# Optimization experiments

Hardware: AMD Instinct MI355X
Metric: run time of the kernel (lower is better)

## Reference

```python
import jax, jax.numpy as jnp
import numpy as np

NUM_HEADS = 16
EPS = 1e-6
CHUNK = 128  # chunk length for exact chunked-recurrent causal linear attention


def setup_inputs() -> dict:
    key = jax.random.key(0)
    ks = jax.random.split(key, 6)
    B, T, E = 4, 2048, 1024
    s = 0.02
    x = jax.random.normal(ks[0], (B, T, E), jnp.float32)
    Wq = jax.random.normal(ks[1], (E, E), jnp.float32) * s
    Wk = jax.random.normal(ks[2], (E, E), jnp.float32) * s
    Wv = jax.random.normal(ks[3], (E, E), jnp.float32) * s
    Wp = jax.random.normal(ks[4], (E, E), jnp.float32) * s
    bp = jnp.zeros((E,), jnp.float32)
    return {"x": x, "Wq": Wq, "Wk": Wk, "Wv": Wv, "Wp": Wp, "bp": bp}


def reference(x, Wq, Wk, Wv, Wp, bp):
    B, T, E = x.shape
    H = NUM_HEADS
    D = E // H
    N = T // CHUNK

    q = x @ Wq.T
    k = x @ Wk.T
    v = x @ Wv.T

    def split_heads(t):  # [B,T,E] -> [B,H,N,C,D]
        return t.reshape(B, T, H, D).transpose(0, 2, 1, 3).reshape(B, H, N, CHUNK, D)

    phi_q = jax.nn.elu(split_heads(q)) + 1.0
    phi_k = jax.nn.elu(split_heads(k)) + 1.0
    vh = split_heads(v)

    # per-chunk KV state and key-sum, then exclusive prefix over chunks
    kv = jnp.einsum('bhncd,bhnce->bhnde', phi_k, vh)        # [B,H,N,D,D]
    zk = phi_k.sum(axis=3)                                   # [B,H,N,D]
    S_prev = jnp.concatenate(
        [jnp.zeros_like(kv[:, :, :1]), jnp.cumsum(kv, axis=2)[:, :, :-1]], axis=2)
    Z_prev = jnp.concatenate(
        [jnp.zeros_like(zk[:, :, :1]), jnp.cumsum(zk, axis=2)[:, :, :-1]], axis=2)

    # intra-chunk causal part
    A = jnp.einsum('bhncd,bhnsd->bhncs', phi_q, phi_k)       # [B,H,N,C,C]
    mask = jnp.tril(jnp.ones((CHUNK, CHUNK), bool))
    A = jnp.where(mask, A, 0.0)

    num = (jnp.einsum('bhncs,bhnse->bhnce', A, vh)
           + jnp.einsum('bhncd,bhnde->bhnce', phi_q, S_prev))
    den = A.sum(-1) + jnp.einsum('bhncd,bhnd->bhnc', phi_q, Z_prev) + EPS
    y = num / den[..., None]                                  # [B,H,N,C,D]

    y = y.reshape(B, H, T, D).transpose(0, 2, 1, 3).reshape(B, T, E)
    return y @ Wp.T + bp
```

## Files before the change

kernel.cpp:

```cpp
#include <hip/hip_runtime.h>
#include <hip/hip_bf16.h>
#include <stdint.h>

#define T_LEN  2048
#define E_DIM  1024
#define BATCH  4
#define HEADS  16
#define HDIM   64
#define CHUNK_ 128
#define NCHUNK 16
#define EPS_   1e-6f

typedef __attribute__((ext_vector_type(8))) short bf16x8;
typedef __attribute__((ext_vector_type(4))) float f32x4;

__device__ __forceinline__ float b2f(__hip_bfloat16 h) { return __bfloat162float(h); }
__device__ __forceinline__ unsigned short f2bu(float f) {
  __hip_bfloat16 h = __float2bfloat16(f);
  return *(unsigned short*)&h;
}
__device__ __forceinline__ void gld_lds16(const void* g, void* l) {
  __builtin_amdgcn_global_load_lds((const __attribute__((address_space(1))) void*)g,
                                   (__attribute__((address_space(3))) void*)l,
                                   16, 0, 0);
}

__global__ __launch_bounds__(256)
void cast5(const float* __restrict__ x,  const float* __restrict__ w0,
           const float* __restrict__ w1, const float* __restrict__ w2,
           const float* __restrict__ w3,
           __hip_bfloat16* __restrict__ xb,  __hip_bfloat16* __restrict__ w0b,
           __hip_bfloat16* __restrict__ w1b, __hip_bfloat16* __restrict__ w2b,
           __hip_bfloat16* __restrict__ w3b)
{
  const int b = blockIdx.x;
  const float* s;
  __hip_bfloat16* d;
  size_t off;
  if (b < 8192) { s = x; d = xb; off = (size_t)b * 1024; }
  else {
    const int i = (b - 8192) >> 10;
    const int r = (b - 8192) & 1023;
    s = (i == 0) ? w0 : (i == 1) ? w1 : (i == 2) ? w2 : w3;
    d = (i == 0) ? w0b : (i == 1) ? w1b : (i == 2) ? w2b : w3b;
    off = (size_t)r * 1024;
  }
  const int t = threadIdx.x;
  float4 v = *(const float4*)(s + off + (size_t)t * 4);
  ushort4 o;
  o.x = f2bu(v.x); o.y = f2bu(v.y); o.z = f2bu(v.z); o.w = f2bu(v.w);
  *(ushort4*)((unsigned short*)d + off + (size_t)t * 4) = o;
}

__device__ __forceinline__ void gemm128_core(
    const __hip_bfloat16* __restrict__ X,
    const __hip_bfloat16* __restrict__ W,
    int bm, int bn, f32x4 acc[4][4],
    __hip_bfloat16* Xs, __hip_bfloat16* Ws)
{
  const int t = threadIdx.x, lane = t & 63, wave = t >> 6;
  const int wm = (wave >> 1) * 64, wn = (wave & 1) * 64;
  for (int k0 = 0; k0 < 1024; k0 += 32) {
    if (k0) __syncthreads();
#pragma unroll
    for (int i = 0; i < 2; ++i) {
      const int j = wave * 2 + i;
      const int m = j * 16 + (lane >> 2);
      const int kg = lane & 3;
      gld_lds16(X + (size_t)(bm * 128 + m) * 1024 + k0 + kg * 8, (char*)Xs + j * 1024);
      gld_lds16(W + (size_t)(bn * 128 + m) * 1024 + k0 + kg * 8, (char*)Ws + j * 1024);
    }
    __syncthreads();
    bf16x8 a[4], b[4];
#pragma unroll
    for (int i = 0; i < 4; ++i) {
      a[i] = *(const bf16x8*)&Xs[((wm + i * 16 + (lane & 15)) * 4 + (lane >> 4)) * 8];
      b[i] = *(const bf16x8*)&Ws[((wn + i * 16 + (lane & 15)) * 4 + (lane >> 4)) * 8];
    }
#pragma unroll
    for (int i = 0; i < 4; ++i)
#pragma unroll
      for (int jn = 0; jn < 4; ++jn)
        acc[i][jn] = __builtin_amdgcn_mfma_f32_16x16x32_bf16(a[i], b[jn], acc[i][jn], 0, 0, 0);
  }
}

__global__ __launch_bounds__(256, 2)
void gemm_qkv(const __hip_bfloat16* __restrict__ X,
              const __hip_bfloat16* __restrict__ Wq,
              const __hip_bfloat16* __restrict__ Wk,
              const __hip_bfloat16* __restrict__ Wv,
              __hip_bfloat16* __restrict__ qo,
              __hip_bfloat16* __restrict__ ko,
              __hip_bfloat16* __restrict__ vo)
{
  __shared__ __align__(16) __hip_bfloat16 Xs[128 * 32];
  __shared__ __align__(16) __hip_bfloat16 Ws[128 * 32];
  const int bm = blockIdx.x, bnx = blockIdx.y;
  const int which = bnx >> 3, bn = bnx & 7;
  const __hip_bfloat16* W = (which == 0) ? Wq : (which == 1) ? Wk : Wv;
  __hip_bfloat16* C = (which == 0) ? qo : (which == 1) ? ko : vo;
  const bool elu = (which < 2);
  f32x4 acc[4][4];
#pragma unroll
  for (int i = 0; i < 4; ++i)
#pragma unroll
    for (int j = 0; j < 4; ++j) acc[i][j] = (f32x4){0.f, 0.f, 0.f, 0.f};
  gemm128_core(X, W, bm, bn, acc, Xs, Ws);
  const int lane = threadIdx.x & 63, wave = threadIdx.x >> 6;
  const int wm = (wave >> 1) * 64, wn = (wave & 1) * 64;
  const int r0 = (lane >> 4) * 4;
#pragma unroll
  for (int mi = 0; mi < 4; ++mi)
#pragma unroll
    for (int ni = 0; ni < 4; ++ni) {
      const int row = bm * 128 + wm + mi * 16 + r0;
      const int col = bn * 128 + wn + ni * 16 + (lane & 15);
#pragma unroll
      for (int r = 0; r < 4; ++r) {
        float v = acc[mi][ni][r];
        if (elu) v = (v > 0.f) ? (v + 1.f) : __expf(v);
        C[(size_t)(row + r) * 1024 + col] = __float2bfloat16(v);
      }
    }
}

__global__ __launch_bounds__(256, 2)
void gemm_out(const __hip_bfloat16* __restrict__ X,
              const __hip_bfloat16* __restrict__ W,
              const float* __restrict__ bias,
              float* __restrict__ C)
{
  __shared__ __align__(16) __hip_bfloat16 Xs[128 * 32];
  __shared__ __align__(16) __hip_bfloat16 Ws[128 * 32];
  const int bm = blockIdx.x, bn = blockIdx.y;
  f32x4 acc[4][4];
#pragma unroll
  for (int i = 0; i < 4; ++i)
#pragma unroll
    for (int j = 0; j < 4; ++j) acc[i][j] = (f32x4){0.f, 0.f, 0.f, 0.f};
  gemm128_core(X, W, bm, bn, acc, Xs, Ws);
  const int lane = threadIdx.x & 63, wave = threadIdx.x >> 6;
  const int wm = (wave >> 1) * 64, wn = (wave & 1) * 64;
  const int r0 = (lane >> 4) * 4;
#pragma unroll
  for (int mi = 0; mi < 4; ++mi)
#pragma unroll
    for (int ni = 0; ni < 4; ++ni) {
      const int row = bm * 128 + wm + mi * 16 + r0;
      const int col = bn * 128 + wn + ni * 16 + (lane & 15);
      const float bv = bias[col];
#pragma unroll
      for (int r = 0; r < 4; ++r)
        C[(size_t)(row + r) * 1024 + col] = acc[mi][ni][r] + bv;
    }
}

__global__ __launch_bounds__(256)
void chunk_kv(const __hip_bfloat16* __restrict__ Kp,
              const __hip_bfloat16* __restrict__ Vp,
              float* __restrict__ kvout, float* __restrict__ zkout,
              unsigned short* __restrict__ vimg)
{
  const int bid = blockIdx.x;
  const int n = bid & 15, h = (bid >> 4) & 15, b = bid >> 8;
  __shared__ __align__(16) __hip_bfloat16 ks[CHUNK_ * HDIM];
  __shared__ __align__(16) __hip_bfloat16 vs[CHUNK_ * HDIM];
  const size_t base = ((size_t)(b * T_LEN + n * CHUNK_)) * E_DIM + h * HDIM;
  const int t = threadIdx.x;
  for (int i = t; i < CHUNK_ * 8; i += 256) {
    int r = i >> 3, c = (i & 7) << 3;
    *(uint4*)&ks[r * HDIM + c] = *(const uint4*)(Kp + base + (size_t)r * E_DIM + c);
    *(uint4*)&vs[r * HDIM + c] = *(const uint4*)(Vp + base + (size_t)r * E_DIM + c);
  }
  __syncthreads();
  const int d0 = (t >> 4) << 2, e0 = (t & 15) << 2;
  float acc[4][4] = {{0.f}};
  float z[4] = {0.f, 0.f, 0.f, 0.f};
  for (int c = 0; c < CHUNK_; ++c) {
    float kv4[4], vv4[4];
#pragma unroll
    for (int i = 0; i < 4; ++i) kv4[i] = b2f(ks[c * HDIM + d0 + i]);
#pragma unroll
    for (int j = 0; j < 4; ++j) vv4[j] = b2f(vs[c * HDIM + e0 + j]);
#pragma unroll
    for (int i = 0; i < 4; ++i) {
      z[i] += kv4[i];
#pragma unroll
      for (int j = 0; j < 4; ++j) acc[i][j] += kv4[i] * vv4[j];
    }
  }
  float* o = kvout + (size_t)bid * (HDIM * HDIM);
  const int dg = d0 >> 3, doff = d0 & 7;
#pragma unroll
  for (int i = 0; i < 4; ++i)
#pragma unroll
    for (int j = 0; j < 4; ++j)
      o[dg * 512 + (e0 + j) * 8 + doff + i] = acc[i][j];
  if (e0 == 0) {
#pragma unroll
    for (int i = 0; i < 4; ++i) zkout[(size_t)bid * HDIM + d0 + i] = z[i];
  }
  const unsigned short* vsu = (const unsigned short*)vs;
  unsigned short* vo = vimg + (size_t)bid * 8192;
  for (int slot = t; slot < 1024; slot += 256) {
    const int sg = slot >> 6, e = slot & 63;
    ushort4 lo, hi;
    lo.x = vsu[(sg * 8 + 0) * 64 + e]; lo.y = vsu[(sg * 8 + 1) * 64 + e];
    lo.z = vsu[(sg * 8 + 2) * 64 + e]; lo.w = vsu[(sg * 8 + 3) * 64 + e];
    hi.x = vsu[(sg * 8 + 4) * 64 + e]; hi.y = vsu[(sg * 8 + 5) * 64 + e];
    hi.z = vsu[(sg * 8 + 6) * 64 + e]; hi.w = vsu[(sg * 8 + 7) * 64 + e];
    *(ushort4*)&vo[slot * 8] = lo;
    *(ushort4*)&vo[slot * 8 + 4] = hi;
  }
}

__global__ __launch_bounds__(256)
void prefix_chunks(float* __restrict__ S, float* __restrict__ Z)
{
  const int bh = blockIdx.x;
  const int t = threadIdx.x;
  float run[16];
#pragma unroll
  for (int j = 0; j < 16; ++j) run[j] = 0.f;
  for (int n = 0; n < NCHUNK; ++n) {
    float* p = S + ((size_t)bh * NCHUNK + n) * (HDIM * HDIM);
#pragma unroll
    for (int j = 0; j < 16; ++j) {
      int idx = t + j * 256;
      float cur = p[idx];
      p[idx] = run[j];
      run[j] += cur;
    }
  }
  if (t < HDIM) {
    float rz = 0.f;
    for (int n = 0; n < NCHUNK; ++n) {
      float* p = Z + ((size_t)bh * NCHUNK + n) * HDIM + t;
      float cur = *p;
      *p = rz;
      rz += cur;
    }
  }
}

#define PW_STRIDE 136

__global__ __launch_bounds__(256, 3)
void chunk_attn(const __hip_bfloat16* __restrict__ Qp,
                const __hip_bfloat16* __restrict__ Kp,
                const unsigned short* __restrict__ vimg,
                const float* __restrict__ Simg,
                const float* __restrict__ Zp,
                __hip_bfloat16* __restrict__ Yp)
{
  __shared__ __align__(16) unsigned short VL[8192];
  __shared__ __align__(16) unsigned short SL[4096];
  __shared__ __align__(16) unsigned short PL[4 * 16 * PW_STRIDE];

  const int bid = blockIdx.x;
  const int n = bid & 15, h = (bid >> 4) & 15, b = bid >> 8;
  const int tokbase = b * T_LEN + n * CHUNK_;
  const size_t gbase = (size_t)tokbase * E_DIM + h * HDIM;
  const int t = threadIdx.x, lane = t & 63, wv = t >> 6;
  const int lm = lane & 15, kg = lane >> 4;

#pragma unroll
  for (int i = 0; i < 4; ++i) {
    const int j = wv * 4 + i;
    gld_lds16(vimg + (size_t)bid * 8192 + (size_t)(j * 64 + lane) * 8,
              (char*)VL + j * 1024);
  }
#pragma unroll
  for (int i = 0; i < 4; ++i) {
    const int idx = i * 1024 + t * 4;
    float4 s4 = *(const float4*)(Simg + (size_t)bid * 4096 + idx);
    ushort4 o;
    o.x = f2bu(s4.x); o.y = f2bu(s4.y); o.z = f2bu(s4.z); o.w = f2bu(s4.w);
    *(ushort4*)&SL[idx] = o;
  }

  const int mts[2] = { wv, 7 - wv };
  bf16x8 aq[2][2];
#pragma unroll
  for (int mi = 0; mi < 2; ++mi)
#pragma unroll
    for (int kh = 0; kh < 2; ++kh)
      aq[mi][kh] = *(const bf16x8*)(Qp + gbase +
                    (size_t)(mts[mi] * 16 + lm) * E_DIM + kh * 32 + kg * 8);
  bf16x8 zb[2];
#pragma unroll
  for (int kh = 0; kh < 2; ++kh) {
    float4 z0 = *(const float4*)(Zp + (size_t)bid * 64 + kh * 32 + kg * 8);
    float4 z1 = *(const float4*)(Zp + (size_t)bid * 64 + kh * 32 + kg * 8 + 4);
    zb[kh][0] = (short)f2bu(z0.x); zb[kh][1] = (short)f2bu(z0.y);
    zb[kh][2] = (short)f2bu(z0.z); zb[kh][3] = (short)f2bu(z0.w);
    zb[kh][4] = (short)f2bu(z1.x); zb[kh][5] = (short)f2bu(z1.y);
    zb[kh][6] = (short)f2bu(z1.z); zb[kh][7] = (short)f2bu(z1.w);
  }

  __syncthreads();

  f32x4 accn[2][4];
  f32x4 accden[2];
#pragma unroll
  for (int mi = 0; mi < 2; ++mi) {
    accden[mi] = (f32x4){EPS_, EPS_, EPS_, EPS_};
#pragma unroll
    for (int ne = 0; ne < 4; ++ne) accn[mi][ne] = (f32x4){0.f, 0.f, 0.f, 0.f};
  }

#pragma unroll
  for (int mi = 0; mi < 2; ++mi)
#pragma unroll
    for (int kh = 0; kh < 2; ++kh) {
      const bf16x8 a = aq[mi][kh];
      accden[mi] = __builtin_amdgcn_mfma_f32_16x16x32_bf16(a, zb[kh], accden[mi], 0, 0, 0);
#pragma unroll
      for (int ne = 0; ne < 4; ++ne) {
        bf16x8 bs = *(const bf16x8*)&SL[((kh * 4 + kg) * 64 + ne * 16 + lm) * 8];
        accn[mi][ne] = __builtin_amdgcn_mfma_f32_16x16x32_bf16(a, bs, accn[mi][ne], 0, 0, 0);
      }
    }

  unsigned short* Pw = PL + wv * 16 * PW_STRIDE;
  bf16x8 ones;
#pragma unroll
  for (int j = 0; j < 8; ++j) ones[j] = (short)0x3F80;

#pragma unroll
  for (int mi = 0; mi < 2; ++mi) {
    const int mt = mts[mi], m0 = mt * 16;
    for (int nt = 0; nt <= mt; ++nt) {
      f32x4 pt = (f32x4){0.f, 0.f, 0.f, 0.f};
#pragma unroll
      for (int kh = 0; kh < 2; ++kh) {
        bf16x8 ak = *(const bf16x8*)(Kp + gbase +
                     (size_t)(nt * 16 + lm) * E_DIM + kh * 32 + kg * 8);
        pt = __builtin_amdgcn_mfma_f32_16x16x32_bf16(ak, aq[mi][kh], pt, 0, 0, 0);
      }
      unsigned short u[4];
#pragma unroll
      for (int r = 0; r < 4; ++r) {
        float v = pt[r];
        if (nt == mt) {
          v = ((kg * 4 + r) <= lm) ? v : 0.f;
        }
        u[r] = f2bu(v);
      }
      const int sidx = lm * PW_STRIDE + nt * 16 + kg * 4;
      *(unsigned*)&Pw[sidx]     = (unsigned)u[0] | ((unsigned)u[1] << 16);
      *(unsigned*)&Pw[sidx + 2] = (unsigned)u[2] | ((unsigned)u[3] << 16);
    }
    if ((mt & 1) == 0 && lane < 32) {
      const int m = lane >> 1, half = lane & 1;
      *(uint4*)&Pw[m * PW_STRIDE + (mt + 1) * 16 + half * 8] = (uint4){0u, 0u, 0u, 0u};
    }
    const int ktc = (mt + 2) >> 1;
    for (int kt = 0; kt < ktc; ++kt) {
      bf16x8 ap = *(const bf16x8*)&Pw[lm * PW_STRIDE + kt * 32 + kg * 8];
      accden[mi] = __builtin_amdgcn_mfma_f32_16x16x32_bf16(ap, ones, accden[mi], 0, 0, 0);
#pragma unroll
      for (int ne = 0; ne < 4; ++ne) {
        bf16x8 bv = *(const bf16x8*)&VL[((kt * 4 + kg) * 64 + ne * 16 + lm) * 8];
        accn[mi][ne] = __builtin_amdgcn_mfma_f32_16x16x32_bf16(ap, bv, accn[mi][ne], 0, 0, 0);
      }
    }
  }

#pragma unroll
  for (int mi = 0; mi < 2; ++mi) {
    const int m0 = mts[mi] * 16;
    float inv[4];
#pragma unroll
    for (int r = 0; r < 4; ++r) inv[r] = 1.f / accden[mi][r];
#pragma unroll
    for (int ne = 0; ne < 4; ++ne) {
      const int col = h * HDIM + ne * 16 + lm;
#pragma unroll
      for (int r = 0; r < 4; ++r) {
        const int row = tokbase + m0 + kg * 4 + r;
        Yp[(size_t)row * E_DIM + col] = __float2bfloat16(accn[mi][ne][r] * inv[r]);
      }
    }
  }
}

extern "C" void kernel_launch(void* const* d_in, const int* in_sizes, int n_in,
                              void* d_out, int out_size, void* d_ws, size_t ws_size,
                              hipStream_t stream)
{
  const float* x  = (const float*)d_in[0];
  const float* Wq = (const float*)d_in[1];
  const float* Wk = (const float*)d_in[2];
  const float* Wv = (const float*)d_in[3];
  const float* Wp = (const float*)d_in[4];
  const float* bp = (const float*)d_in[5];
  float* out = (float*)d_out;

  const size_t MT = (size_t)BATCH * T_LEN;
  char* w = (char*)d_ws;
  __hip_bfloat16* xb  = (__hip_bfloat16*)w; w += MT * E_DIM * sizeof(__hip_bfloat16);
  __hip_bfloat16* Wqb = (__hip_bfloat16*)w; w += (size_t)E_DIM * E_DIM * sizeof(__hip_bfloat16);
  __hip_bfloat16* Wkb = (__hip_bfloat16*)w; w += (size_t)E_DIM * E_DIM * sizeof(__hip_bfloat16);
  __hip_bfloat16* Wvb = (__hip_bfloat16*)w; w += (size_t)E_DIM * E_DIM * sizeof(__hip_bfloat16);
  __hip_bfloat16* Wpb = (__hip_bfloat16*)w; w += (size_t)E_DIM * E_DIM * sizeof(__hip_bfloat16);
  __hip_bfloat16* q = (__hip_bfloat16*)w; w += MT * E_DIM * sizeof(__hip_bfloat16);
  __hip_bfloat16* k = (__hip_bfloat16*)w; w += MT * E_DIM * sizeof(__hip_bfloat16);
  __hip_bfloat16* v = (__hip_bfloat16*)w; w += MT * E_DIM * sizeof(__hip_bfloat16);
  __hip_bfloat16* y = (__hip_bfloat16*)w; w += MT * E_DIM * sizeof(__hip_bfloat16);
  float* S = (float*)w; w += (size_t)BATCH * HEADS * NCHUNK * HDIM * HDIM * sizeof(float);
  float* Z = (float*)w; w += (size_t)BATCH * HEADS * NCHUNK * HDIM * sizeof(float);
  unsigned short* vimg = (unsigned short*)xb;

  cast5<<<8192 + 4096, 256, 0, stream>>>(x, Wq, Wk, Wv, Wp, xb, Wqb, Wkb, Wvb, Wpb);
  gemm_qkv<<<dim3(MT / 128, 24), 256, 0, stream>>>(xb, Wqb, Wkb, Wvb, q, k, v);
  chunk_kv<<<BATCH * HEADS * NCHUNK, 256, 0, stream>>>(k, v, S, Z, vimg);
  prefix_chunks<<<BATCH * HEADS, 256, 0, stream>>>(S, Z);
  chunk_attn<<<BATCH * HEADS * NCHUNK, 256, 0, stream>>>(q, k, vimg, S, Z, y);
  gemm_out<<<dim3(MT / 128, 8), 256, 0, stream>>>(y, Wpb, bp, out);
}
```

Before: 246.7 us.

## Replace QKV GEMM with 256x256-tile double-buffered pipelined MFMA kernel

Replaces the 128x128-tile QKV projection GEMM with a 512-thread kernel using 256x256 output tiles and BK=64. It double-buffers LDS with swizzled layouts, interleaves quarter-tile global-to-LDS loads with MFMA phases using explicit vmcnt waits and barriers, and raises wave priority during MFMA blocks. The aim is more data reuse per tile and hiding global load latency behind compute. The cost is 128KB of LDS per block and fewer blocks (384) to spread across the CUs.

New measurement: 260.0 us. 5.4% more time.

```diff
diff --git a/kernel.cpp b/kernel.cpp
--- a/kernel.cpp
+++ b/kernel.cpp
@@ -85,44 +85,207 @@
   }
 }
 
-__global__ __launch_bounds__(256, 2)
-void gemm_qkv(const __hip_bfloat16* __restrict__ X,
-              const __hip_bfloat16* __restrict__ Wq,
-              const __hip_bfloat16* __restrict__ Wk,
-              const __hip_bfloat16* __restrict__ Wv,
-              __hip_bfloat16* __restrict__ qo,
-              __hip_bfloat16* __restrict__ ko,
-              __hip_bfloat16* __restrict__ vo)
-{
-  __shared__ __align__(16) __hip_bfloat16 Xs[128 * 32];
-  __shared__ __align__(16) __hip_bfloat16 Ws[128 * 32];
-  const int bm = blockIdx.x, bnx = blockIdx.y;
-  const int which = bnx >> 3, bn = bnx & 7;
-  const __hip_bfloat16* W = (which == 0) ? Wq : (which == 1) ? Wk : Wv;
+__global__ __launch_bounds__(512, 2)
+void gemm_qkv_256(const __hip_bfloat16* __restrict__ X,
+                  const __hip_bfloat16* __restrict__ Wq,
+                  const __hip_bfloat16* __restrict__ Wk,
+                  const __hip_bfloat16* __restrict__ Wv,
+                  __hip_bfloat16* __restrict__ qo,
+                  __hip_bfloat16* __restrict__ ko,
+                  __hip_bfloat16* __restrict__ vo)
+{
+  __shared__ __align__(16) unsigned short As[2][16384];
+  __shared__ __align__(16) unsigned short Bs[2][16384];
+
+  const int bm = blockIdx.x;
+  const int byy = blockIdx.y;
+  const int which = byy >> 2, bn = byy & 3;
+  const __hip_bfloat16* Wsel = (which == 0) ? Wq : (which == 1) ? Wk : Wv;
   __hip_bfloat16* C = (which == 0) ? qo : (which == 1) ? ko : vo;
   const bool elu = (which < 2);
-  f32x4 acc[4][4];
-#pragma unroll
-  for (int i = 0; i < 4; ++i)
-#pragma unroll
-    for (int j = 0; j < 4; ++j) acc[i][j] = (f32x4){0.f, 0.f, 0.f, 0.f};
-  gemm128_core(X, W, bm, bn, acc, Xs, Ws);
-  const int lane = threadIdx.x & 63, wave = threadIdx.x >> 6;
-  const int wm = (wave >> 1) * 64, wn = (wave & 1) * 64;
+
+  const int t = threadIdx.x, lane = t & 63, wv = t >> 6;
+  const int wm = (wv >> 2) * 128;
+  const int wn = (wv & 3) * 64;
+
+  const __hip_bfloat16* Xp = X + (size_t)(bm * 256) * 1024;
+  const __hip_bfloat16* Wp = Wsel + (size_t)(bn * 256) * 1024;
+
+  const int lo    = (lane & 15) * 128;
+  const int lohi0 = lo + (((lane >> 4)    ) ^ (lane & 7)) * 16;
+  const int lohi1 = lo + (((lane >> 4) | 4) ^ (lane & 7)) * 16;
+
+  auto stage_half = [&](int jn, int c) {
+    if (jn >= 16) return;
+    const int buf = jn & 1;
+    const int k0 = jn * 64;
+#pragma unroll
+    for (int ci = 0; ci < 2; ++ci) {
+      const int i = wv * 2 + ci;
+      int row0;
+      const __hip_bfloat16* G;
+      char* L;
+      if (c == 0)      { row0 = (i & 7) * 8 + (i >> 3) * 128;      G = Xp; L = (char*)&As[buf][0]; }
+      else if (c == 2) { row0 = 64 + (i & 7) * 8 + (i >> 3) * 128; G = Xp; L = (char*)&As[buf][0]; }
+      else if (c == 1) { row0 = (i & 3) * 8 + (i >> 2) * 64;       G = Wp; L = (char*)&Bs[buf][0]; }
+      else             { row0 = 32 + (i & 3) * 8 + (i >> 2) * 64;  G = Wp; L = (char*)&Bs[buf][0]; }
+      const int row = row0 + (lane >> 3);
+      const int cg  = (lane & 7) ^ (lane >> 3);
+      gld_lds16(G + (size_t)row * 1024 + k0 + cg * 8, L + row0 * 128);
+    }
+  };
+
+  auto vmw = [&](int n) {
+    if (n == 6)      asm volatile("s_waitcnt vmcnt(6)" ::: "memory");
+    else if (n == 4) asm volatile("s_waitcnt vmcnt(4)" ::: "memory");
+    else if (n == 2) asm volatile("s_waitcnt vmcnt(2)" ::: "memory");
+    else             asm volatile("s_waitcnt vmcnt(0)" ::: "memory");
+  };
+
+  f32x4 acc[8][4];
+#pragma unroll
+  for (int m = 0; m < 8; ++m)
+#pragma unroll
+    for (int n = 0; n < 4; ++n) acc[m][n] = (f32x4){0.f, 0.f, 0.f, 0.f};
+
+  bf16x8 a0[4][2], a1[4][2], b0[2][2], b1[2][2];
+  {
+    bf16x8 zz;
+#pragma unroll
+    for (int i = 0; i < 8; ++i) zz[i] = (short)0;
+#pragma unroll
+    for (int m = 0; m < 4; ++m) { a1[m][0] = zz; a1[m][1] = zz; }
+#pragma unroll
+    for (int n = 0; n < 2; ++n) { b1[n][0] = zz; b1[n][1] = zz; }
+  }
+
+  stage_half(0, 0); stage_half(0, 1); stage_half(0, 2); stage_half(0, 3);
+  vmw(6);
+  __builtin_amdgcn_s_barrier();
+
+  auto kstep = [&](int j, int buf, bool last) {
+    const char* Ab = (const char*)&As[buf][0];
+    const char* Bb = (const char*)&Bs[buf][0];
+    const int jn = j + 1;
+
+#pragma unroll
+    for (int m = 0; m < 4; ++m) {
+      a0[m][0] = *(const bf16x8*)(Ab + (wm + m * 16) * 128 + lohi0);
+      a0[m][1] = *(const bf16x8*)(Ab + (wm + m * 16) * 128 + lohi1);
+    }
+    stage_half(jn, 0);
+    __builtin_amdgcn_s_barrier();
+    asm volatile("s_waitcnt lgkmcnt(0)" ::: "memory");
+    __builtin_amdgcn_sched_barrier(0);
+    __builtin_amdgcn_s_setprio(1);
+#pragma unroll
+    for (int m = 0; m < 4; ++m)
+#pragma unroll
+      for (int n = 0; n < 2; ++n) {
+        acc[4 + m][2 + n] = __builtin_amdgcn_mfma_f32_16x16x32_bf16(a1[m][0], b1[n][0], acc[4 + m][2 + n], 0, 0, 0);
+        acc[4 + m][2 + n] = __builtin_amdgcn_mfma_f32_16x16x32_bf16(a1[m][1], b1[n][1], acc[4 + m][2 + n], 0, 0, 0);
+      }
+    __builtin_amdgcn_s_setprio(0);
+    vmw(last ? 4 : 6);
+    __builtin_amdgcn_s_barrier();
+
+#pragma unroll
+    for (int n = 0; n < 2; ++n) {
+      b0[n][0] = *(const bf16x8*)(Bb + (wn + n * 16) * 128 + lohi0);
+      b0[n][1] = *(const bf16x8*)(Bb + (wn + n * 16) * 128 + lohi1);
+    }
+    stage_half(jn, 1);
+    __builtin_amdgcn_s_barrier();
+    asm volatile("s_waitcnt lgkmcnt(0)" ::: "memory");
+    __builtin_amdgcn_sched_barrier(0);
+    __builtin_amdgcn_s_setprio(1);
+#pragma unroll
+    for (int m = 0; m < 4; ++m)
+#pragma unroll
+      for (int n = 0; n < 2; ++n) {
+        acc[m][n] = __builtin_amdgcn_mfma_f32_16x16x32_bf16(a0[m][0], b0[n][0], acc[m][n], 0, 0, 0);
+        acc[m][n] = __builtin_amdgcn_mfma_f32_16x16x32_bf16(a0[m][1], b0[n][1], acc[m][n], 0, 0, 0);
+      }
+    __builtin_amdgcn_s_setprio(0);
+    vmw(last ? 2 : 6);
+    __builtin_amdgcn_s_barrier();
+
+#pragma unroll
+    for (int m = 0; m < 4; ++m) {
+      a1[m][0] = *(const bf16x8*)(Ab + (wm + 64 + m * 16) * 128 + lohi0);
+      a1[m][1] = *(const bf16x8*)(Ab + (wm + 64 + m * 16) * 128 + lohi1);
+    }
+    stage_half(jn, 2);
+    __builtin_amdgcn_s_barrier();
+    asm volatile("s_waitcnt lgkmcnt(0)" ::: "memory");
+    __builtin_amdgcn_sched_barrier(0);
+    __builtin_amdgcn_s_setprio(1);
+#pragma unroll
+    for (int m = 0; m < 4; ++m)
+#pragma unroll
+      for (int n = 0; n < 2; ++n) {
+        acc[4 + m][n] = __builtin_amdgcn_mfma_f32_16x16x32_bf16(a1[m][0], b0[n][0], acc[4 + m][n], 0, 0, 0);
+        acc[4 + m][n] = __builtin_amdgcn_mfma_f32_16x16x32_bf16(a1[m][1], b0[n][1], acc[4 + m][n], 0, 0, 0);
+      }
+    __builtin_amdgcn_s_setprio(0);
+    vmw(last ? 0 : 6);
+    __builtin_amdgcn_s_barrier();
+
+#pragma unroll
+    for (int n = 0; n < 2; ++n) {
+      b1[n][0] = *(const bf16x8*)(Bb + (wn + 32 + n * 16) * 128 + lohi0);
+      b1[n][1] = *(const bf16x8*)(Bb + (wn + 32 + n * 16) * 128 + lohi1);
+    }
+    stage_half(jn, 3);
+    __builtin_amdgcn_s_barrier();
+    asm volatile("s_waitcnt lgkmcnt(0)" ::: "memory");
+    __builtin_amdgcn_sched_barrier(0);
+    __builtin_amdgcn_s_setprio(1);
+#pragma unroll
+    for (int m = 0; m < 4; ++m)
+#pragma unroll
+      for (int n = 0; n < 2; ++n) {
+        acc[m][2 + n] = __builtin_amdgcn_mfma_f32_16x16x32_bf16(a0[m][0], b1[n][0], acc[m][2 + n], 0, 0, 0);
+        acc[m][2 + n] = __builtin_amdgcn_mfma_f32_16x16x32_bf16(a0[m][1], b1[n][1], acc[m][2 + n], 0, 0, 0);
+      }
+    __builtin_amdgcn_s_setprio(0);
+    if (!last) {
+      vmw(6);
+      __builtin_amdgcn_s_barrier();
+    }
+  };
+
+#pragma unroll 1
+  for (int jj = 0; jj < 7; ++jj) {
+    kstep(2 * jj,     0, false);
+    kstep(2 * jj + 1, 1, false);
+  }
+  kstep(14, 0, false);
+  kstep(15, 1, true);
+
+#pragma unroll
+  for (int m = 0; m < 4; ++m)
+#pragma unroll
+    for (int n = 0; n < 2; ++n) {
+      acc[4 + m][2 + n] = __builtin_amdgcn_mfma_f32_16x16x32_bf16(a1[m][0], b1[n][0], acc[4 + m][2 + n], 0, 0, 0);
+      acc[4 + m][2 + n] = __builtin_amdgcn_mfma_f32_16x16x32_bf16(a1[m][1], b1[n][1], acc[4 + m][2 + n], 0, 0, 0);
+    }
+
   const int r0 = (lane >> 4) * 4;
 #pragma unroll
-  for (int mi = 0; mi < 4; ++mi)
-#pragma unroll
-    for (int ni = 0; ni < 4; ++ni) {
-      const int row = bm * 128 + wm + mi * 16 + r0;
-      const int col = bn * 128 + wn + ni * 16 + (lane & 15);
+  for (int m = 0; m < 8; ++m) {
+    const int row = bm * 256 + wm + m * 16 + r0;
+#pragma unroll
+    for (int n = 0; n < 4; ++n) {
+      const int col = bn * 256 + wn + n * 16 + (lane & 15);
 #pragma unroll
       for (int r = 0; r < 4; ++r) {
-        float v = acc[mi][ni][r];
-        if (elu) v = (v > 0.f) ? (v + 1.f) : __expf(v);
-        C[(size_t)(row + r) * 1024 + col] = __float2bfloat16(v);
-      }
-    }
+        float vv = acc[m][n][r];
+        if (elu) vv = (vv > 0.f) ? (vv + 1.f) : __expf(vv);
+        C[(size_t)(row + r) * 1024 + col] = __float2bfloat16(vv);
+      }
+    }
+  }
 }
 
 __global__ __launch_bounds__(256, 2)
@@ -414,7 +577,7 @@
   unsigned short* vimg = (unsigned short*)xb;
 
   cast5<<<8192 + 4096, 256, 0, stream>>>(x, Wq, Wk, Wv, Wp, xb, Wqb, Wkb, Wvb, Wpb);
-  gemm_qkv<<<dim3(MT / 128, 24), 256, 0, stream>>>(xb, Wqb, Wkb, Wvb, q, k, v);
+  gemm_qkv_256<<<dim3(32, 12), 512, 0, stream>>>(xb, Wqb, Wkb, Wvb, q, k, v);
   chunk_kv<<<BATCH * HEADS * NCHUNK, 256, 0, stream>>>(k, v, S, Z, vimg);
   prefix_chunks<<<BATCH * HEADS, 256, 0, stream>>>(S, Z);
   chunk_attn<<<BATCH * HEADS * NCHUNK, 256, 0, stream>>>(q, k, vimg, S, Z, y);
```

## Rewrite QKV GEMM with 128x256 tiles, triple-buffered LDS pipeline and swizzle

Applied to the files above, without the earlier changes.

Replaces the QKV projection GEMM with a 512-thread kernel that computes 128x256 output tiles with a K-step of 64. Global-to-LDS loads go into three LDS buffers and are interleaved between MFMA groups, with explicit vmcnt waits, s_setprio and register double-buffering of fragments. An XOR swizzle on the LDS layout is meant to avoid bank conflicts. The goal is to hide memory latency and raise MFMA utilisation, at the cost of heavy LDS use (about 144KB) and a single block per CU.

After: 245.6 us. Within noise of the previous version (-0.4%).

```diff
diff --git a/kernel.cpp b/kernel.cpp
--- a/kernel.cpp
+++ b/kernel.cpp
@@ -24,6 +24,8 @@
                                    (__attribute__((address_space(3))) void*)l,
                                    16, 0, 0);
 }
+
+#define MFMA16(a, b, c) __builtin_amdgcn_mfma_f32_16x16x32_bf16((a), (b), (c), 0, 0, 0)
 
 __global__ __launch_bounds__(256)
 void cast5(const float* __restrict__ x,  const float* __restrict__ w0,
@@ -81,48 +83,187 @@
     for (int i = 0; i < 4; ++i)
 #pragma unroll
       for (int jn = 0; jn < 4; ++jn)
-        acc[i][jn] = __builtin_amdgcn_mfma_f32_16x16x32_bf16(a[i], b[jn], acc[i][jn], 0, 0, 0);
-  }
-}
-
-__global__ __launch_bounds__(256, 2)
-void gemm_qkv(const __hip_bfloat16* __restrict__ X,
-              const __hip_bfloat16* __restrict__ Wq,
-              const __hip_bfloat16* __restrict__ Wk,
-              const __hip_bfloat16* __restrict__ Wv,
-              __hip_bfloat16* __restrict__ qo,
-              __hip_bfloat16* __restrict__ ko,
-              __hip_bfloat16* __restrict__ vo)
-{
-  __shared__ __align__(16) __hip_bfloat16 Xs[128 * 32];
-  __shared__ __align__(16) __hip_bfloat16 Ws[128 * 32];
-  const int bm = blockIdx.x, bnx = blockIdx.y;
-  const int which = bnx >> 3, bn = bnx & 7;
-  const __hip_bfloat16* W = (which == 0) ? Wq : (which == 1) ? Wk : Wv;
-  __hip_bfloat16* C = (which == 0) ? qo : (which == 1) ? ko : vo;
+        acc[i][jn] = MFMA16(a[i], b[jn], acc[i][jn]);
+  }
+}
+
+__global__ __launch_bounds__(512, 1)
+void gemm_qkv_v2(const __hip_bfloat16* __restrict__ X,
+                 const __hip_bfloat16* __restrict__ Wq,
+                 const __hip_bfloat16* __restrict__ Wk,
+                 const __hip_bfloat16* __restrict__ Wv,
+                 __hip_bfloat16* __restrict__ qo,
+                 __hip_bfloat16* __restrict__ ko,
+                 __hip_bfloat16* __restrict__ vo)
+{
+  __shared__ __align__(16) unsigned short As[3][8192];
+  __shared__ __align__(16) unsigned short Bs[3][16384];
+
+  const int bm = blockIdx.x;
+  const int byy = blockIdx.y;
+  const int which = byy >> 2, bn = byy & 3;
+  const __hip_bfloat16* Wsel = (which == 0) ? Wq : (which == 1) ? Wk : Wv;
+  __hip_bfloat16* Cc = (which == 0) ? qo : (which == 1) ? ko : vo;
   const bool elu = (which < 2);
+
+  const int t = threadIdx.x, lane = t & 63, wv = t >> 6;
+  const int wm = (wv >> 2) * 64;
+  const int wn = (wv & 3) * 64;
+
+  const __hip_bfloat16* Xp = X + (size_t)(bm * 128) * 1024;
+  const __hip_bfloat16* Wp = Wsel + (size_t)(bn * 256) * 1024;
+
+  const int lo    = (lane & 15) * 128;
+  const int lohi0 = lo + (((lane >> 4)    ) ^ (lane & 7)) * 16;
+  const int lohi1 = lo + (((lane >> 4) | 4) ^ (lane & 7)) * 16;
+  const int srow = lane >> 3;
+  const int scg  = (lane & 7) ^ (lane >> 3);
+
+  auto stA = [&](int buf, int k0) {
+#pragma unroll
+    for (int ci = 0; ci < 2; ++ci) {
+      const int row0 = (wv * 2 + ci) * 8;
+      gld_lds16(Xp + (size_t)(row0 + srow) * 1024 + k0 + scg * 8,
+                (char*)&As[buf][0] + row0 * 128);
+    }
+  };
+  auto stB0 = [&](int buf, int k0) {
+#pragma unroll
+    for (int ci = 0; ci < 2; ++ci) {
+      const int row0 = (wv * 2 + ci) * 8;
+      gld_lds16(Wp + (size_t)(row0 + srow) * 1024 + k0 + scg * 8,
+                (char*)&Bs[buf][0] + row0 * 128);
+    }
+  };
+  auto stB1 = [&](int buf, int k0) {
+#pragma unroll
+    for (int ci = 0; ci < 2; ++ci) {
+      const int row0 = 128 + (wv * 2 + ci) * 8;
+      gld_lds16(Wp + (size_t)(row0 + srow) * 1024 + k0 + scg * 8,
+                (char*)&Bs[buf][0] + row0 * 128);
+    }
+  };
+  auto rdA = [&](int buf, int half, bf16x8 (&d)[2][2]) {
+#pragma unroll
+    for (int m = 0; m < 2; ++m) {
+      const int rb = wm + half * 32 + m * 16;
+      d[m][0] = *(const bf16x8*)((const char*)&As[buf][0] + rb * 128 + lohi0);
+      d[m][1] = *(const bf16x8*)((const char*)&As[buf][0] + rb * 128 + lohi1);
+    }
+  };
+  auto rdB = [&](int buf, int half, bf16x8 (&d)[2][2]) {
+#pragma unroll
+    for (int n = 0; n < 2; ++n) {
+      const int rb = wn + half * 32 + n * 16;
+      d[n][0] = *(const bf16x8*)((const char*)&Bs[buf][0] + rb * 128 + lohi0);
+      d[n][1] = *(const bf16x8*)((const char*)&Bs[buf][0] + rb * 128 + lohi1);
+    }
+  };
+
   f32x4 acc[4][4];
 #pragma unroll
-  for (int i = 0; i < 4; ++i)
-#pragma unroll
-    for (int j = 0; j < 4; ++j) acc[i][j] = (f32x4){0.f, 0.f, 0.f, 0.f};
-  gemm128_core(X, W, bm, bn, acc, Xs, Ws);
-  const int lane = threadIdx.x & 63, wave = threadIdx.x >> 6;
-  const int wm = (wave >> 1) * 64, wn = (wave & 1) * 64;
+  for (int m = 0; m < 4; ++m)
+#pragma unroll
+    for (int n = 0; n < 4; ++n) acc[m][n] = (f32x4){0.f, 0.f, 0.f, 0.f};
+
+  bf16x8 Aa01[2][2], Ab01[2][2], Aa23[2][2], Ab23[2][2];
+  bf16x8 Ba01[2][2], Bb01[2][2], Ba23[2][2], Bb23[2][2];
+
+  stA(0, 0);  stB0(0, 0);  stB1(0, 0);
+  stA(1, 64); stB0(1, 64); stB1(1, 64);
+  asm volatile("s_waitcnt vmcnt(6)" ::: "memory");
+  __builtin_amdgcn_s_barrier();
+  __builtin_amdgcn_sched_barrier(0);
+  rdA(0, 0, Aa01); rdB(0, 0, Ab01); rdA(0, 1, Aa23); rdB(0, 1, Ab23);
+
+  auto qstep = [&](int j, int c,
+                   bf16x8 (&ca01)[2][2], bf16x8 (&cb01)[2][2],
+                   bf16x8 (&ca23)[2][2], bf16x8 (&cb23)[2][2],
+                   bf16x8 (&na01)[2][2], bf16x8 (&nb01)[2][2],
+                   bf16x8 (&na23)[2][2], bf16x8 (&nb23)[2][2]) {
+    const int stg  = (c + 2 >= 3) ? c - 1 : c + 2;
+    const int nbuf = (c + 1 >= 3) ? 0 : c + 1;
+    const int k0n  = (j + 2) * 64;
+    const bool dost = (j < 14);
+
+    __builtin_amdgcn_s_setprio(1);
+#pragma unroll
+    for (int m = 0; m < 2; ++m)
+#pragma unroll
+      for (int n = 0; n < 2; ++n) {
+        acc[m][n] = MFMA16(ca01[m][0], cb01[n][0], acc[m][n]);
+        acc[m][n] = MFMA16(ca01[m][1], cb01[n][1], acc[m][n]);
+      }
+    __builtin_amdgcn_s_setprio(0);
+    if (dost) stA(stg, k0n);
+
+    __builtin_amdgcn_s_setprio(1);
+#pragma unroll
+    for (int m = 0; m < 2; ++m)
+#pragma unroll
+      for (int n = 0; n < 2; ++n) {
+        acc[m][2 + n] = MFMA16(ca01[m][0], cb23[n][0], acc[m][2 + n]);
+        acc[m][2 + n] = MFMA16(ca01[m][1], cb23[n][1], acc[m][2 + n]);
+      }
+    __builtin_amdgcn_s_setprio(0);
+    if (dost) stB0(stg, k0n);
+
+    __builtin_amdgcn_s_setprio(1);
+#pragma unroll
+    for (int m = 0; m < 2; ++m)
+#pragma unroll
+      for (int n = 0; n < 2; ++n) {
+        acc[2 + m][n] = MFMA16(ca23[m][0], cb01[n][0], acc[2 + m][n]);
+        acc[2 + m][n] = MFMA16(ca23[m][1], cb01[n][1], acc[2 + m][n]);
+      }
+    __builtin_amdgcn_s_setprio(0);
+    if (dost) stB1(stg, k0n);
+
+    if (j == 14) asm volatile("s_waitcnt vmcnt(0)" ::: "memory");
+    else         asm volatile("s_waitcnt vmcnt(6)" ::: "memory");
+    __builtin_amdgcn_s_barrier();
+    __builtin_amdgcn_sched_barrier(0);
+
+    rdA(nbuf, 0, na01); rdB(nbuf, 0, nb01);
+
+    __builtin_amdgcn_s_setprio(1);
+#pragma unroll
+    for (int m = 0; m < 2; ++m)
+#pragma unroll
+      for (int n = 0; n < 2; ++n) {
+        acc[2 + m][2 + n] = MFMA16(ca23[m][0], cb23[n][0], acc[2 + m][2 + n]);
+        acc[2 + m][2 + n] = MFMA16(ca23[m][1], cb23[n][1], acc[2 + m][2 + n]);
+      }
+    __builtin_amdgcn_s_setprio(0);
+
+    rdA(nbuf, 1, na23); rdB(nbuf, 1, nb23);
+  };
+
+  int c = 0;
+#pragma unroll 1
+  for (int jj = 0; jj < 8; ++jj) {
+    qstep(2 * jj, c, Aa01, Ab01, Aa23, Ab23, Ba01, Bb01, Ba23, Bb23);
+    c = (c == 2) ? 0 : c + 1;
+    qstep(2 * jj + 1, c, Ba01, Bb01, Ba23, Bb23, Aa01, Ab01, Aa23, Ab23);
+    c = (c == 2) ? 0 : c + 1;
+  }
+
+  const int lm = lane & 15;
   const int r0 = (lane >> 4) * 4;
 #pragma unroll
-  for (int mi = 0; mi < 4; ++mi)
-#pragma unroll
-    for (int ni = 0; ni < 4; ++ni) {
-      const int row = bm * 128 + wm + mi * 16 + r0;
-      const int col = bn * 128 + wn + ni * 16 + (lane & 15);
+  for (int m = 0; m < 4; ++m) {
+    const int row = bm * 128 + wm + m * 16 + r0;
+#pragma unroll
+    for (int n = 0; n < 4; ++n) {
+      const int col = bn * 256 + wn + n * 16 + lm;
 #pragma unroll
       for (int r = 0; r < 4; ++r) {
-        float v = acc[mi][ni][r];
-        if (elu) v = (v > 0.f) ? (v + 1.f) : __expf(v);
-        C[(size_t)(row + r) * 1024 + col] = __float2bfloat16(v);
-      }
-    }
+        float vv = acc[m][n][r];
+        if (elu) vv = (vv > 0.f) ? (vv + 1.f) : __expf(vv);
+        Cc[(size_t)(row + r) * 1024 + col] = __float2bfloat16(vv);
+      }
+    }
+  }
 }
 
 __global__ __launch_bounds__(256, 2)
@@ -315,11 +456,11 @@
 #pragma unroll
     for (int kh = 0; kh < 2; ++kh) {
       const bf16x8 a = aq[mi][kh];
-      accden[mi] = __builtin_amdgcn_mfma_f32_16x16x32_bf16(a, zb[kh], accden[mi], 0, 0, 0);
+      accden[mi] = MFMA16(a, zb[kh], accden[mi]);
 #pragma unroll
       for (int ne = 0; ne < 4; ++ne) {
         bf16x8 bs = *(const bf16x8*)&SL[((kh * 4 + kg) * 64 + ne * 16 + lm) * 8];
-        accn[mi][ne] = __builtin_amdgcn_mfma_f32_16x16x32_bf16(a, bs, accn[mi][ne], 0, 0, 0);
+        accn[mi][ne] = MFMA16(a, bs, accn[mi][ne]);
       }
     }
 
@@ -337,7 +478,7 @@
       for (int kh = 0; kh < 2; ++kh) {
         bf16x8 ak = *(const bf16x8*)(Kp + gbase +
                      (size_t)(nt * 16 + lm) * E_DIM + kh * 32 + kg * 8);
-        pt = __builtin_amdgcn_mfma_f32_16x16x32_bf16(ak, aq[mi][kh], pt, 0, 0, 0);
+        pt = MFMA16(ak, aq[mi][kh], pt);
       }
       unsigned short u[4];
 #pragma unroll
@@ -359,11 +500,11 @@
     const int ktc = (mt + 2) >> 1;
     for (int kt = 0; kt < ktc; ++kt) {
       bf16x8 ap = *(const bf16x8*)&Pw[lm * PW_STRIDE + kt * 32 + kg * 8];
-      accden[mi] = __builtin_amdgcn_mfma_f32_16x16x32_bf16(ap, ones, accden[mi], 0, 0, 0);
+      accden[mi] = MFMA16(ap, ones, accden[mi]);
 #pragma unroll
       for (int ne = 0; ne < 4; ++ne) {
         bf16x8 bv = *(const bf16x8*)&VL[((kt * 4 + kg) * 64 + ne * 16 + lm) * 8];
-        accn[mi][ne] = __builtin_amdgcn_mfma_f32_16x16x32_bf16(ap, bv, accn[mi][ne], 0, 0, 0);
+        accn[mi][ne] = MFMA16(ap, bv, accn[mi][ne]);
       }
     }
   }
@@ -414,7 +555,7 @@
   unsigned short* vimg = (unsigned short*)xb;
 
   cast5<<<8192 + 4096, 256, 0, stream>>>(x, Wq, Wk, Wv, Wp, xb, Wqb, Wkb, Wvb, Wpb);
-  gemm_qkv<<<dim3(MT / 128, 24), 256, 0, stream>>>(xb, Wqb, Wkb, Wvb, q, k, v);
+  gemm_qkv_v2<<<dim3(64, 12), 512, 0, stream>>>(xb, Wqb, Wkb, Wvb, q, k, v);
   chunk_kv<<<BATCH * HEADS * NCHUNK, 256, 0, stream>>>(k, v, S, Z, vimg);
   prefix_chunks<<<BATCH * HEADS, 256, 0, stream>>>(S, Z);
   chunk_attn<<<BATCH * HEADS * NCHUNK, 256, 0, stream>>>(q, k, vimg, S, Z, y);
```
